# Kernel tuning notes

Measured on AMD Instinct MI355X. Metric: run time of the kernel, lower is better.

Reference implementation:

```python
import jax, jax.numpy as jnp
import numpy as np

K_NN = 9
HEADS = 4
SCALE = 2
NUM_CLASSES = 10
BATCH = 256


def pixel_unshuffle(x, s):
    # x: [B, C, H, W] -> [B, C*s*s, H/s, W/s] (torch PixelUnshuffle channel order)
    B, C, H, W = x.shape
    x = x.reshape(B, C, H // s, s, W // s, s)
    return x.transpose(0, 1, 3, 5, 2, 4).reshape(B, C * s * s, H // s, W // s)


def pixel_shuffle(x, s):
    # x: [B, C, H, W] -> [B, C/(s*s), H*s, W*s]
    B, C, H, W = x.shape
    c = C // (s * s)
    x = x.reshape(B, c, s, s, H, W)
    return x.transpose(0, 1, 4, 2, 5, 3).reshape(B, c, H * s, W * s)


def convnn_branch_layer(x, Wc, bc, Wq, Wk, Wv, Wo, bo):
    # Attention_ConvNN_Random_Branching (samples='all', shuffle_pattern='BA'):
    # pixel-unshuffle -> tokens -> [local 1x1-conv branch | KNN attention branch] -> concat -> 1x1 proj -> pixel-shuffle
    x = pixel_unshuffle(x, SCALE)               # [B, Cu, h, w]
    B, Cu, h, w = x.shape
    N = h * w
    t = x.reshape(B, Cu, N).transpose(0, 2, 1)  # [B, N, Cu] tokens

    local = jax.nn.relu(t @ Wc + bc)            # [B, N, r0] local (pointwise) branch

    q = t @ Wq                                  # [B, N, d]
    k = t @ Wk
    v = t @ Wv
    d = q.shape[-1]
    dh = d // HEADS

    # K-nearest-neighbor selection over ALL tokens by q/k similarity
    sim = jnp.einsum('bnd,bmd->bnm', q, k)      # [B, N, N]
    _, idx = jax.lax.top_k(sim, K_NN)           # [B, N, K]

    gather = jax.vmap(lambda a, i: a[i])        # per-batch neighbor gather
    k_nb = gather(k, idx)                       # [B, N, K, d]
    v_nb = gather(v, idx)                       # [B, N, K, d]

    qh = q.reshape(B, N, HEADS, dh)
    k_nbh = k_nb.reshape(B, N, K_NN, HEADS, dh)
    v_nbh = v_nb.reshape(B, N, K_NN, HEADS, dh)

    scale = jnp.asarray(1.0 / np.sqrt(dh), q.dtype)
    logits = jnp.einsum('bnhd,bnkhd->bnhk', qh, k_nbh) * scale  # [B, N, H, K]
    attn = jax.nn.softmax(logits, axis=-1)
    agg = jnp.einsum('bnhk,bnkhd->bnhd', attn, v_nbh).reshape(B, N, d)

    out = jnp.concatenate([local, agg], axis=-1) @ Wo + bo      # [B, N, Co]
    out = out.transpose(0, 2, 1).reshape(B, -1, h, w)
    return pixel_shuffle(out, SCALE)            # [B, out_ch, H, W]


def setup_inputs() -> dict:
    key = jax.random.key(0)
    ks = jax.random.split(key, 20)

    def w(k, shape, fan_in):
        return (jax.random.normal(k, shape, dtype=jnp.float32) / np.sqrt(fan_in)).astype(jnp.float32)

    # layer 1: in_ch=3 -> Cu=12, branches (16,16), out_ch=16 -> Co=64
    Cu1, r1, d1, Co1 = 12, 16, 16, 64
    # layer 2: in_ch=16 -> Cu=64, branches (32,32), out_ch=32 -> Co=128
    Cu2, r2, d2, Co2 = 64, 32, 32, 128

    inp = {
        'x': jax.random.normal(ks[0], (BATCH, 3, 32, 32), dtype=jnp.float32),
        'w1c': w(ks[1], (Cu1, r1), Cu1), 'b1c': jnp.zeros((r1,), jnp.float32),
        'w1q': w(ks[2], (Cu1, d1), Cu1), 'w1k': w(ks[3], (Cu1, d1), Cu1), 'w1v': w(ks[4], (Cu1, d1), Cu1),
        'w1o': w(ks[5], (r1 + d1, Co1), r1 + d1), 'b1o': jnp.zeros((Co1,), jnp.float32),
        'w2c': w(ks[6], (Cu2, r2), Cu2), 'b2c': jnp.zeros((r2,), jnp.float32),
        'w2q': w(ks[7], (Cu2, d2), Cu2), 'w2k': w(ks[8], (Cu2, d2), Cu2), 'w2v': w(ks[9], (Cu2, d2), Cu2),
        'w2o': w(ks[10], (r2 + d2, Co2), r2 + d2), 'b2o': jnp.zeros((Co2,), jnp.float32),
        'fc1_w': w(ks[11], (32768, 1024), 32768), 'fc1_b': jnp.zeros((1024,), jnp.float32),
        'fc2_w': w(ks[12], (1024, NUM_CLASSES), 1024), 'fc2_b': jnp.zeros((NUM_CLASSES,), jnp.float32),
    }
    return inp


def reference(x, w1c, b1c, w1q, w1k, w1v, w1o, b1o,
              w2c, b2c, w2q, w2k, w2v, w2o, b2o,
              fc1_w, fc1_b, fc2_w, fc2_b):
    h = convnn_branch_layer(x, w1c, b1c, w1q, w1k, w1v, w1o, b1o)   # [B, 16, 32, 32]
    h = convnn_branch_layer(h, w2c, b2c, w2q, w2k, w2v, w2o, b2o)   # [B, 32, 32, 32]
    h = h.reshape(h.shape[0], -1)                                   # [B, 32768]
    h = jax.nn.relu(h @ fc1_w + fc1_b)
    return h @ fc2_w + fc2_b                                        # [B, 10]
```

## Files before the change

### kernel.cpp

```cpp
#include <hip/hip_runtime.h>
#include <math.h>


typedef float floatx4 __attribute__((ext_vector_type(4)));
typedef __bf16 bf16x8 __attribute__((ext_vector_type(8)));

static constexpr size_t OQ1 = 0;
static constexpr size_t OK1 = 1048576;
static constexpr size_t OV1 = 2097152;
static constexpr size_t OL1 = 3145728;
static constexpr size_t OA1 = 4194304;
static constexpr size_t OT2 = 5242880;
static constexpr size_t OQ2 = 0;
static constexpr size_t OK2 = 2097152;
static constexpr size_t OV2 = 9437184;
static constexpr size_t OL2 = 11534336;
static constexpr size_t OA2 = 13631488;
static constexpr size_t OH  = 5242880;
static constexpr size_t OPART = 9437184;

__device__ inline bf16x8 pack8(const float* f) {
  bf16x8 v;
#pragma unroll
  for (int i = 0; i < 8; ++i) v[i] = (__bf16)f[i];
  return v;
}

__global__ __launch_bounds__(256) void k1_qkv1(
    const float* __restrict__ x, const float* __restrict__ w1q,
    const float* __restrict__ w1k, const float* __restrict__ w1v,
    const float* __restrict__ w1c, const float* __restrict__ b1c,
    float* __restrict__ q1, float* __restrict__ k1,
    float* __restrict__ v1, float* __restrict__ loc1)
{
  const int tid = threadIdx.x;
  const int slot = tid >> 6;
  const int lane = tid & 63;
  const int tok = blockIdx.x * 4 + slot;
  const int b = tok >> 8, n = tok & 255;
  const int i = n >> 4, j = n & 15;
  __shared__ float ts[4][12];
  if (lane < 12) {
    const int c0 = lane >> 2, si = (lane >> 1) & 1, sj = lane & 1;
    ts[slot][lane] = x[((size_t)(b * 3 + c0) * 32 + 2 * i + si) * 32 + 2 * j + sj];
  }
  __syncthreads();
  const int mat = lane >> 4, col = lane & 15;
  const float* W = (mat == 0) ? w1q : (mat == 1) ? w1k : (mat == 2) ? w1v : w1c;
  float acc = 0.f;
#pragma unroll
  for (int c = 0; c < 12; ++c) acc += ts[slot][c] * W[c * 16 + col];
  const size_t o = (size_t)tok * 16 + col;
  if (mat == 0) q1[o] = acc;
  else if (mat == 1) k1[o] = acc;
  else if (mat == 2) v1[o] = acc;
  else loc1[o] = fmaxf(acc + b1c[col], 0.f);
}

template <int D, int DH, int NH>
__global__ __launch_bounds__(256) void attn_sel(
    const float* __restrict__ q, const float* __restrict__ k,
    const float* __restrict__ v, float* __restrict__ agg)
{
  constexpr int KS_BYTES = 256 * D * 4;
  constexpr int MERGE_BYTES = 9216 + 9216 + 2304;
  constexpr int SMEM_BYTES = (KS_BYTES > MERGE_BYTES) ? KS_BYTES : MERGE_BYTES;
  __shared__ __align__(16) char smem[SMEM_BYTES];
  float* ks  = (float*)smem;
  float* mvS = (float*)smem;
  int*   miS = (int*)(smem + 9216);
  int*   selS = (int*)(smem + 18432);

  const int blk = blockIdx.x;
  const int b = blk >> 2;
  const int t0 = (blk & 3) * 64;
  const int tid = threadIdx.x;
  const int tok = tid & 63;
  const int qt = tid >> 6;
  const size_t base = (size_t)b * (256 * D);
  for (int idx = tid * 4; idx < 256 * D; idx += 1024)
    *(float4*)&ks[idx] = *(const float4*)&k[base + idx];
  float qr[D];
  {
    const float4* qrow = (const float4*)&q[base + (size_t)(t0 + tok) * D];
#pragma unroll
    for (int c4 = 0; c4 < D / 4; ++c4) {
      const float4 qv = qrow[c4];
      qr[4 * c4 + 0] = qv.x; qr[4 * c4 + 1] = qv.y;
      qr[4 * c4 + 2] = qv.z; qr[4 * c4 + 3] = qv.w;
    }
  }
  __syncthreads();

  float topv[9];
  int topi[9];
#pragma unroll
  for (int r = 0; r < 9; ++r) { topv[r] = -__builtin_inff(); topi[r] = 0; }

#pragma unroll 2
  for (int j = 0; j < 64; ++j) {
    const int m = qt * 64 + j;
    const float4* kr = (const float4*)&ks[m * D];
    float p0 = 0.f, p1 = 0.f, p2 = 0.f, p3 = 0.f;
#pragma unroll
    for (int g = 0; g < D / 16; ++g) {
      const float4 ka = kr[g * 4 + 0], kb = kr[g * 4 + 1];
      const float4 kc = kr[g * 4 + 2], kd = kr[g * 4 + 3];
      p0 += qr[g*16+ 0]*ka.x + qr[g*16+ 1]*ka.y + qr[g*16+ 2]*ka.z + qr[g*16+ 3]*ka.w;
      p1 += qr[g*16+ 4]*kb.x + qr[g*16+ 5]*kb.y + qr[g*16+ 6]*kb.z + qr[g*16+ 7]*kb.w;
      p2 += qr[g*16+ 8]*kc.x + qr[g*16+ 9]*kc.y + qr[g*16+10]*kc.z + qr[g*16+11]*kc.w;
      p3 += qr[g*16+12]*kd.x + qr[g*16+13]*kd.y + qr[g*16+14]*kd.z + qr[g*16+15]*kd.w;
    }
    const float s = (p0 + p1) + (p2 + p3);
    bool ci = s > topv[8];
#pragma unroll
    for (int i = 8; i >= 1; --i) {
      const bool cim1 = s > topv[i - 1];
      topv[i] = ci ? (cim1 ? topv[i - 1] : s) : topv[i];
      topi[i] = ci ? (cim1 ? topi[i - 1] : m) : topi[i];
      ci = cim1;
    }
    topv[0] = ci ? s : topv[0];
    topi[0] = ci ? m : topi[0];
  }
  __syncthreads();
#pragma unroll
  for (int r = 0; r < 9; ++r) {
    mvS[qt * 576 + tok * 9 + r] = topv[r];
    miS[qt * 576 + tok * 9 + r] = topi[r];
  }
  __syncthreads();
  if (qt == 0) {
    float fv[9];
    int fi[9];
#pragma unroll
    for (int r = 0; r < 9; ++r) { fv[r] = -__builtin_inff(); fi[r] = 0; }
#pragma unroll
    for (int qq = 0; qq < 4; ++qq)
#pragma unroll
      for (int r = 0; r < 9; ++r) {
        const float s = mvS[qq * 576 + tok * 9 + r];
        const int ix = miS[qq * 576 + tok * 9 + r];
        bool ci = s > fv[8];
#pragma unroll
        for (int i = 8; i >= 1; --i) {
          const bool cim1 = s > fv[i - 1];
          fv[i] = ci ? (cim1 ? fv[i - 1] : s) : fv[i];
          fi[i] = ci ? (cim1 ? fi[i - 1] : ix) : fi[i];
          ci = cim1;
        }
        fv[0] = ci ? s : fv[0];
        fi[0] = ci ? ix : fi[0];
      }
#pragma unroll
    for (int r = 0; r < 9; ++r) selS[tok * 9 + r] = fi[r];
  }
  __syncthreads();

  const int hh = qt;
  const float scale = (DH == 4) ? 0.5f : 0.35355339059327373f;
  int sel9[9];
#pragma unroll
  for (int kk = 0; kk < 9; ++kk) sel9[kk] = selS[tok * 9 + kk];
  float lg9[9];
#pragma unroll
  for (int kk = 0; kk < 9; ++kk) {
    const float4* kr = (const float4*)&k[base + (size_t)sel9[kk] * D + hh * DH];
    float s = 0.f;
#pragma unroll
    for (int u = 0; u < DH / 4; ++u) {
      const float4 ka = kr[u];
      s += qr[hh*DH + u*4 + 0]*ka.x + qr[hh*DH + u*4 + 1]*ka.y +
           qr[hh*DH + u*4 + 2]*ka.z + qr[hh*DH + u*4 + 3]*ka.w;
    }
    lg9[kk] = s * scale;
  }
  float mx = lg9[0];
#pragma unroll
  for (int kk = 1; kk < 9; ++kk) mx = fmaxf(mx, lg9[kk]);
  float sum = 0.f;
#pragma unroll
  for (int kk = 0; kk < 9; ++kk) { lg9[kk] = __expf(lg9[kk] - mx); sum += lg9[kk]; }
  const float inv = 1.f / sum;
  float oacc[DH];
#pragma unroll
  for (int c = 0; c < DH; ++c) oacc[c] = 0.f;
#pragma unroll
  for (int kk = 0; kk < 9; ++kk) {
    const float4* vr = (const float4*)&v[base + (size_t)sel9[kk] * D + hh * DH];
    const float w = lg9[kk] * inv;
#pragma unroll
    for (int u = 0; u < DH / 4; ++u) {
      const float4 va = vr[u];
      oacc[u*4+0] += w * va.x; oacc[u*4+1] += w * va.y;
      oacc[u*4+2] += w * va.z; oacc[u*4+3] += w * va.w;
    }
  }
  float* o = &agg[base + (size_t)(t0 + tok) * D + hh * DH];
#pragma unroll
  for (int u = 0; u < DH / 4; ++u)
    *(float4*)&o[u * 4] = make_float4(oacc[u*4], oacc[u*4+1], oacc[u*4+2], oacc[u*4+3]);
}

__global__ __launch_bounds__(256) void proj1(
    const float* __restrict__ loc1, const float* __restrict__ agg1,
    const float* __restrict__ w1o, const float* __restrict__ b1o,
    float* __restrict__ t2)
{
  const int tid = threadIdx.x;
  const int tok = blockIdx.x * 256 + tid;
  __shared__ float wS[32 * 64];
  __shared__ float bS[64];
  for (int idx = tid * 4; idx < 2048; idx += 1024)
    *(float4*)&wS[idx] = *(const float4*)&w1o[idx];
  if (tid < 64) bS[tid] = b1o[tid];
  float cat[32];
#pragma unroll
  for (int c4 = 0; c4 < 4; ++c4) {
    const float4 l4 = *(const float4*)&loc1[(size_t)tok * 16 + c4 * 4];
    cat[4*c4+0] = l4.x; cat[4*c4+1] = l4.y; cat[4*c4+2] = l4.z; cat[4*c4+3] = l4.w;
    const float4 a4 = *(const float4*)&agg1[(size_t)tok * 16 + c4 * 4];
    cat[16+4*c4+0] = a4.x; cat[16+4*c4+1] = a4.y; cat[16+4*c4+2] = a4.z; cat[16+4*c4+3] = a4.w;
  }
  __syncthreads();
  float acc[64];
#pragma unroll
  for (int o = 0; o < 64; ++o) acc[o] = 0.f;
#pragma unroll 4
  for (int c = 0; c < 32; ++c) {
    const float cv = cat[c];
#pragma unroll
    for (int o4 = 0; o4 < 16; ++o4) {
      const float4 w4 = *(const float4*)&wS[c * 64 + o4 * 4];
      acc[o4*4+0] += cv * w4.x; acc[o4*4+1] += cv * w4.y;
      acc[o4*4+2] += cv * w4.z; acc[o4*4+3] += cv * w4.w;
    }
  }
  float* dst = t2 + (size_t)tok * 64;
#pragma unroll
  for (int o4 = 0; o4 < 16; ++o4)
    *(float4*)&dst[o4 * 4] = make_float4(acc[o4*4] + bS[o4*4], acc[o4*4+1] + bS[o4*4+1],
                                         acc[o4*4+2] + bS[o4*4+2], acc[o4*4+3] + bS[o4*4+3]);
}

__global__ __launch_bounds__(256) void k4_qkv2(
    const float* __restrict__ t2, const float* __restrict__ w2q,
    const float* __restrict__ w2k, const float* __restrict__ w2v,
    const float* __restrict__ w2c, const float* __restrict__ b2c,
    float* __restrict__ q2, float* __restrict__ k2,
    float* __restrict__ v2, float* __restrict__ loc2)
{
  const int blk = blockIdx.x;
  const int tid = threadIdx.x;
  __shared__ float t2S[64 * 68];
  __shared__ float wS[4 * 2312];
  __shared__ float bS[32];
  for (int idx = tid * 4; idx < 4096; idx += 1024) {
    const float4 vv = *(const float4*)&t2[(size_t)blk * 4096 + idx];
    *(float4*)&t2S[(idx >> 6) * 68 + (idx & 63)] = vv;
  }
  for (int idx = tid * 4; idx < 2048; idx += 1024) {
    const int c = idx >> 5, col = idx & 31;
    *(float4*)&wS[0 * 2312 + c * 36 + col] = *(const float4*)&w2q[idx];
    *(float4*)&wS[1 * 2312 + c * 36 + col] = *(const float4*)&w2k[idx];
    *(float4*)&wS[2 * 2312 + c * 36 + col] = *(const float4*)&w2v[idx];
    *(float4*)&wS[3 * 2312 + c * 36 + col] = *(const float4*)&w2c[idx];
  }
  if (tid < 32) bS[tid] = b2c[tid];
  __syncthreads();
  const int tq = tid >> 2, mat = tid & 3;
  const float* wm = &wS[mat * 2312];
  float acc[32];
#pragma unroll
  for (int e = 0; e < 32; ++e) acc[e] = 0.f;
#pragma unroll 4
  for (int c = 0; c < 64; ++c) {
    const float tv = t2S[tq * 68 + c];
#pragma unroll
    for (int o4 = 0; o4 < 8; ++o4) {
      const float4 w4 = *(const float4*)&wm[c * 36 + o4 * 4];
      acc[o4*4+0] += tv * w4.x; acc[o4*4+1] += tv * w4.y;
      acc[o4*4+2] += tv * w4.z; acc[o4*4+3] += tv * w4.w;
    }
  }
  if (mat == 3) {
#pragma unroll
    for (int e = 0; e < 32; ++e) acc[e] = fmaxf(acc[e] + bS[e], 0.f);
  }
  float* dst = (mat == 0) ? q2 : (mat == 1) ? k2 : (mat == 2) ? v2 : loc2;
  float* drow = dst + (size_t)(blk * 64 + tq) * 32;
#pragma unroll
  for (int o4 = 0; o4 < 8; ++o4)
    *(float4*)&drow[o4 * 4] = make_float4(acc[o4*4], acc[o4*4+1], acc[o4*4+2], acc[o4*4+3]);
}

__global__ __launch_bounds__(256) void proj2h(
    const float* __restrict__ loc2, const float* __restrict__ agg2,
    const float* __restrict__ w2o, const float* __restrict__ b2o,
    __bf16* __restrict__ h)
{
  const int b = blockIdx.x;
  const int t = threadIdx.x;
  __shared__ __bf16 catB[256 * 72];
  __shared__ __bf16 wB[128 * 72];
  {
    const int n = t >> 1, khalf = t & 1;
    float wv[32];
#pragma unroll
    for (int j = 0; j < 32; ++j) wv[j] = w2o[(size_t)(khalf * 32 + j) * 128 + n];
#pragma unroll
    for (int j8 = 0; j8 < 4; ++j8)
      *(bf16x8*)&wB[n * 72 + khalf * 32 + j8 * 8] = pack8(&wv[j8 * 8]);
  }
  {
    float lv[32];
#pragma unroll
    for (int c4 = 0; c4 < 8; ++c4) {
      const float4 x4 = *(const float4*)&loc2[(size_t)(b * 256 + t) * 32 + c4 * 4];
      lv[4*c4+0] = x4.x; lv[4*c4+1] = x4.y; lv[4*c4+2] = x4.z; lv[4*c4+3] = x4.w;
    }
#pragma unroll
    for (int c8 = 0; c8 < 4; ++c8)
      *(bf16x8*)&catB[t * 72 + c8 * 8] = pack8(&lv[c8 * 8]);
#pragma unroll
    for (int c4 = 0; c4 < 8; ++c4) {
      const float4 x4 = *(const float4*)&agg2[(size_t)(b * 256 + t) * 32 + c4 * 4];
      lv[4*c4+0] = x4.x; lv[4*c4+1] = x4.y; lv[4*c4+2] = x4.z; lv[4*c4+3] = x4.w;
    }
#pragma unroll
    for (int c8 = 0; c8 < 4; ++c8)
      *(bf16x8*)&catB[t * 72 + 32 + c8 * 8] = pack8(&lv[c8 * 8]);
  }
  __syncthreads();
  const int w = t >> 6, lane = t & 63, qd = lane >> 4, mcol = lane & 15;
#pragma unroll
  for (int nc = 0; nc < 2; ++nc) {
    floatx4 acc[4][4];
#pragma unroll
    for (int mi = 0; mi < 4; ++mi)
#pragma unroll
      for (int nj = 0; nj < 4; ++nj) acc[mi][nj] = (floatx4)0.f;
#pragma unroll
    for (int s = 0; s < 2; ++s) {
      bf16x8 af[4], bf[4];
#pragma unroll
      for (int mi = 0; mi < 4; ++mi)
        af[mi] = *(const bf16x8*)&catB[(w * 64 + mi * 16 + mcol) * 72 + s * 32 + qd * 8];
#pragma unroll
      for (int nj = 0; nj < 4; ++nj)
        bf[nj] = *(const bf16x8*)&wB[((nc * 4 + nj) * 16 + mcol) * 72 + s * 32 + qd * 8];
#pragma unroll
      for (int mi = 0; mi < 4; ++mi)
#pragma unroll
        for (int nj = 0; nj < 4; ++nj)
          acc[mi][nj] = __builtin_amdgcn_mfma_f32_16x16x32_bf16(af[mi], bf[nj], acc[mi][nj], 0, 0, 0);
    }
#pragma unroll
    for (int mi = 0; mi < 4; ++mi)
#pragma unroll
      for (int nj = 0; nj < 4; ++nj) {
        const int ch = (nc * 4 + nj) * 16 + mcol;
        const float bb = b2o[ch];
        const int cc = ch >> 2, si = (ch >> 1) & 1, sj = ch & 1;
#pragma unroll
        for (int r = 0; r < 4; ++r) {
          const int tok = w * 64 + mi * 16 + qd * 4 + r;
          const int i = tok >> 4, j = tok & 15;
          h[(size_t)b * 32768 + cc * 1024 + (2 * i + si) * 32 + (2 * j + sj)] =
              (__bf16)(acc[mi][nj][r] + bb);
        }
      }
  }
}

__global__ __launch_bounds__(256) void k7_fc1_gemm(
    const __bf16* __restrict__ A,
    const float* __restrict__ Bw,
    float* __restrict__ part)
{
  __shared__ __bf16 Bs[32 * 264];
  const int bn = blockIdx.x & 31;
  const int bk = blockIdx.x >> 5;
  const int n0 = bn * 32, k0 = bk * 2048;
  const int tid = threadIdx.x;
  const int n = tid & 31;
  const int kg = tid >> 5;
  const int w = tid >> 6, lane = tid & 63;
  const int qd = lane >> 4, mcol = lane & 15;
  floatx4 acc[4][2];
#pragma unroll
  for (int mi = 0; mi < 4; ++mi)
#pragma unroll
    for (int ni = 0; ni < 2; ++ni) acc[mi][ni] = (floatx4)0.f;

  for (int it = 0; it < 8; ++it) {
    const int kk0 = k0 + it * 256;
    float bv[32];
    const float* bp = Bw + (size_t)(kk0 + kg * 32) * 1024 + n0 + n;
#pragma unroll
    for (int j = 0; j < 32; ++j) bv[j] = bp[(size_t)j * 1024];
    __syncthreads();
#pragma unroll
    for (int j8 = 0; j8 < 4; ++j8)
      *(bf16x8*)&Bs[n * 264 + kg * 32 + j8 * 8] = pack8(&bv[j8 * 8]);
    __syncthreads();
#pragma unroll
    for (int s = 0; s < 8; ++s) {
      bf16x8 af[4], bf[2];
#pragma unroll
      for (int mi = 0; mi < 4; ++mi)
        af[mi] = *(const bf16x8*)(A + (size_t)(w * 64 + mi * 16 + mcol) * 32768
                                     + kk0 + s * 32 + qd * 8);
#pragma unroll
      for (int ni = 0; ni < 2; ++ni)
        bf[ni] = *(const bf16x8*)&Bs[(ni * 16 + mcol) * 264 + s * 32 + qd * 8];
#pragma unroll
      for (int mi = 0; mi < 4; ++mi)
#pragma unroll
        for (int ni = 0; ni < 2; ++ni)
          acc[mi][ni] = __builtin_amdgcn_mfma_f32_16x16x32_bf16(af[mi], bf[ni], acc[mi][ni], 0, 0, 0);
    }
  }
  float* P = part + (size_t)bk * 262144;
#pragma unroll
  for (int mi = 0; mi < 4; ++mi)
#pragma unroll
    for (int ni = 0; ni < 2; ++ni) {
      const int col = n0 + ni * 16 + mcol;
#pragma unroll
      for (int r = 0; r < 4; ++r) {
        const int row = w * 64 + mi * 16 + qd * 4 + r;
        P[(size_t)row * 1024 + col] = acc[mi][ni][r];
      }
    }
}

__global__ __launch_bounds__(256) void k7c8_fc2(
    const float* __restrict__ part, const float* __restrict__ fc1b,
    const float* __restrict__ w2, const float* __restrict__ b2,
    float* __restrict__ out)
{
  const int b = blockIdx.x, t = threadIdx.x;
  const int col4 = t * 4;
  float4 s = make_float4(0.f, 0.f, 0.f, 0.f);
#pragma unroll
  for (int p = 0; p < 16; ++p) {
    const float4 x4 = *(const float4*)&part[(size_t)p * 262144 + (size_t)b * 1024 + col4];
    s.x += x4.x; s.y += x4.y; s.z += x4.z; s.w += x4.w;
  }
  const float4 bb = *(const float4*)&fc1b[col4];
  float a[4] = {fmaxf(s.x + bb.x, 0.f), fmaxf(s.y + bb.y, 0.f),
                fmaxf(s.z + bb.z, 0.f), fmaxf(s.w + bb.w, 0.f)};
  float acc[10];
#pragma unroll
  for (int o = 0; o < 10; ++o) acc[o] = 0.f;
#pragma unroll
  for (int i = 0; i < 4; ++i) {
    const float* wr = w2 + (size_t)(col4 + i) * 10;
#pragma unroll
    for (int o = 0; o < 10; ++o) acc[o] += a[i] * wr[o];
  }
  __shared__ float red[256][10];
#pragma unroll
  for (int o = 0; o < 10; ++o) red[t][o] = acc[o];
  __syncthreads();
  for (int st = 128; st > 0; st >>= 1) {
    if (t < st) {
#pragma unroll
      for (int o = 0; o < 10; ++o) red[t][o] += red[t + st][o];
    }
    __syncthreads();
  }
  if (t < 10) out[b * 10 + t] = red[0][t] + b2[t];
}

extern "C" void kernel_launch(void* const* d_in, const int* in_sizes, int n_in,
                              void* d_out, int out_size, void* d_ws, size_t ws_size,
                              hipStream_t stream)
{
  const float* x    = (const float*)d_in[0];
  const float* w1c  = (const float*)d_in[1];
  const float* b1c  = (const float*)d_in[2];
  const float* w1q  = (const float*)d_in[3];
  const float* w1k  = (const float*)d_in[4];
  const float* w1v  = (const float*)d_in[5];
  const float* w1o  = (const float*)d_in[6];
  const float* b1o  = (const float*)d_in[7];
  const float* w2c  = (const float*)d_in[8];
  const float* b2c  = (const float*)d_in[9];
  const float* w2q  = (const float*)d_in[10];
  const float* w2k  = (const float*)d_in[11];
  const float* w2v  = (const float*)d_in[12];
  const float* w2o  = (const float*)d_in[13];
  const float* b2o  = (const float*)d_in[14];
  const float* fc1w = (const float*)d_in[15];
  const float* fc1b = (const float*)d_in[16];
  const float* fc2w = (const float*)d_in[17];
  const float* fc2b = (const float*)d_in[18];
  float* out = (float*)d_out;
  float* ws = (float*)d_ws;

  float* q1   = ws + OQ1;
  float* k1   = ws + OK1;
  float* v1   = ws + OV1;
  float* loc1 = ws + OL1;
  float* agg1 = ws + OA1;
  float* t2   = ws + OT2;
  float* q2   = ws + OQ2;
  float* k2   = ws + OK2;
  float* v2   = ws + OV2;
  float* loc2 = ws + OL2;
  float* agg2 = ws + OA2;
  __bf16* h   = (__bf16*)(ws + OH);
  float* prt  = ws + OPART;

  k1_qkv1<<<16384, 256, 0, stream>>>(x, w1q, w1k, w1v, w1c, b1c, q1, k1, v1, loc1);
  attn_sel<16, 4, 4><<<1024, 256, 0, stream>>>(q1, k1, v1, agg1);
  proj1<<<256, 256, 0, stream>>>(loc1, agg1, w1o, b1o, t2);
  k4_qkv2<<<1024, 256, 0, stream>>>(t2, w2q, w2k, w2v, w2c, b2c, q2, k2, v2, loc2);
  attn_sel<32, 8, 4><<<1024, 256, 0, stream>>>(q2, k2, v2, agg2);
  proj2h<<<256, 256, 0, stream>>>(loc2, agg2, w2o, b2o, h);
  k7_fc1_gemm<<<512, 256, 0, stream>>>(h, fc1w, prt);
  k7c8_fc2<<<256, 256, 0, stream>>>(prt, fc1b, fc2w, fc2b, out);
}
```

Before: 475.0 us.

## Stage fc1 A tiles through LDS with register prefetch of next K-chunk

The fc1 GEMM kernel now copies the activation tile into shared memory with coalesced 16-byte loads instead of having each wave read A fragments directly from global memory. The K step per iteration shrinks from 256 to 64, and the next chunk of A and of the weight matrix is prefetched into registers while the MFMAs on the current chunk run. The aim is to hide global-load latency and improve coalescing of the A reads. In exchange the kernel uses more registers and LDS, and makes four times as many passes, each with two barriers.

```diff
diff --git a/kernel.cpp b/kernel.cpp
--- a/kernel.cpp
+++ b/kernel.cpp
@@ -378,12 +378,15 @@
     const float* __restrict__ Bw,
     float* __restrict__ part)
 {
-  __shared__ __bf16 Bs[32 * 264];
+  __shared__ __bf16 As[256 * 72];
+  __shared__ __bf16 Bs[32 * 72];
   const int bn = blockIdx.x & 31;
   const int bk = blockIdx.x >> 5;
   const int n0 = bn * 32, k0 = bk * 2048;
   const int tid = threadIdx.x;
-  const int n = tid & 31;
+  const int ar = tid >> 3;
+  const int ac = tid & 7;
+  const int nb = tid & 31;
   const int kg = tid >> 5;
   const int w = tid >> 6, lane = tid & 63;
   const int qd = lane >> 4, mcol = lane & 15;
@@ -393,27 +396,45 @@
 #pragma unroll
     for (int ni = 0; ni < 2; ++ni) acc[mi][ni] = (floatx4)0.f;
 
-  for (int it = 0; it < 8; ++it) {
-    const int kk0 = k0 + it * 256;
-    float bv[32];
-    const float* bp = Bw + (size_t)(kk0 + kg * 32) * 1024 + n0 + n;
-#pragma unroll
-    for (int j = 0; j < 32; ++j) bv[j] = bp[(size_t)j * 1024];
+  uint4 apf[8];
+  float bpf[8];
+#pragma unroll
+  for (int l = 0; l < 8; ++l)
+    apf[l] = *(const uint4*)(A + (size_t)(ar + l * 32) * 32768 + k0 + ac * 8);
+#pragma unroll
+  for (int j = 0; j < 8; ++j)
+    bpf[j] = Bw[(size_t)(k0 + kg * 8 + j) * 1024 + n0 + nb];
+
+  for (int it = 0; it < 32; ++it) {
     __syncthreads();
 #pragma unroll
-    for (int j8 = 0; j8 < 4; ++j8)
-      *(bf16x8*)&Bs[n * 264 + kg * 32 + j8 * 8] = pack8(&bv[j8 * 8]);
+    for (int l = 0; l < 8; ++l)
+      *(uint4*)&As[(ar + l * 32) * 72 + ac * 8] = apf[l];
+    {
+      float tmp[8];
+#pragma unroll
+      for (int j = 0; j < 8; ++j) tmp[j] = bpf[j];
+      *(bf16x8*)&Bs[nb * 72 + kg * 8] = pack8(tmp);
+    }
     __syncthreads();
-#pragma unroll
-    for (int s = 0; s < 8; ++s) {
+    if (it < 31) {
+      const int kn = k0 + (it + 1) * 64;
+#pragma unroll
+      for (int l = 0; l < 8; ++l)
+        apf[l] = *(const uint4*)(A + (size_t)(ar + l * 32) * 32768 + kn + ac * 8);
+#pragma unroll
+      for (int j = 0; j < 8; ++j)
+        bpf[j] = Bw[(size_t)(kn + kg * 8 + j) * 1024 + n0 + nb];
+    }
+#pragma unroll
+    for (int s = 0; s < 2; ++s) {
       bf16x8 af[4], bf[2];
 #pragma unroll
       for (int mi = 0; mi < 4; ++mi)
-        af[mi] = *(const bf16x8*)(A + (size_t)(w * 64 + mi * 16 + mcol) * 32768
-                                     + kk0 + s * 32 + qd * 8);
+        af[mi] = *(const bf16x8*)&As[(w * 64 + mi * 16 + mcol) * 72 + s * 32 + qd * 8];
 #pragma unroll
       for (int ni = 0; ni < 2; ++ni)
-        bf[ni] = *(const bf16x8*)&Bs[(ni * 16 + mcol) * 264 + s * 32 + qd * 8];
+        bf[ni] = *(const bf16x8*)&Bs[(ni * 16 + mcol) * 72 + s * 32 + qd * 8];
 #pragma unroll
       for (int mi = 0; mi < 4; ++mi)
 #pragma unroll
```

Result: slower. 590.3 us (+24.3%).
